# Performance work log

Hardware: AMD Instinct MI355X
Metric: run time of the kernel (lower is better)

## Reference

```python
import jax, jax.numpy as jnp
import numpy as np

E, D, A = 1024, 1024, 512

def setup_inputs() -> dict:
    key = jax.random.key(0)
    ks = jax.random.split(key, 8)
    B, S = 32, 2048
    s_e = 1.0 / np.sqrt(E)
    s_d = 1.0 / np.sqrt(D)
    s_a = 1.0 / np.sqrt(A)
    return {
        "encoder_outputs": jax.random.normal(ks[0], (B, S, E), jnp.float32),
        "decoder_hidden": jax.random.normal(ks[1], (B, D), jnp.float32),
        "We": jax.random.uniform(ks[2], (E, A), jnp.float32, -s_e, s_e),
        "be": jax.random.uniform(ks[3], (A,), jnp.float32, -s_e, s_e),
        "Wd": jax.random.uniform(ks[4], (D, A), jnp.float32, -s_d, s_d),
        "bd": jax.random.uniform(ks[5], (A,), jnp.float32, -s_d, s_d),
        "v_w": jax.random.uniform(ks[6], (A,), jnp.float32, -s_a, s_a),
        "v_b": jax.random.uniform(ks[7], (), jnp.float32, -s_a, s_a),
    }

def reference(encoder_outputs, decoder_hidden, We, be, Wd, bd, v_w, v_b):
    # encoder_energy: [B,S,A]; decoder_energy: [B,1,A]
    enc_e = jnp.einsum('bse,ea->bsa', encoder_outputs, We) + be
    dec_e = (decoder_hidden @ Wd + bd)[:, None, :]
    energy = jnp.tanh(enc_e + dec_e)                     # [B,S,A]
    scores = jnp.einsum('bsa,a->bs', energy, v_w) + v_b  # [B,S]
    attn = jax.nn.softmax(scores, axis=1)                # [B,S]
    context = jnp.einsum('bs,bse->be', attn, encoder_outputs)  # [B,E]
    return context, attn
```

## Files before the change

### kernel.cpp

```cpp
#include <hip/hip_runtime.h>
#include <math.h>

#define E_DIM 1024
#define D_DIM 1024
#define A_DIM 512
#define B_NUM 32
#define S_DIM 2048
#define M_DIM (B_NUM * S_DIM)

typedef unsigned short ushort;
typedef short short8 __attribute__((ext_vector_type(8)));
typedef float f32x4 __attribute__((ext_vector_type(4)));
typedef unsigned short ushort4v __attribute__((ext_vector_type(4)));
typedef unsigned int uint2v __attribute__((ext_vector_type(2)));

typedef const void __attribute__((address_space(1))) cglobal_t;
typedef void __attribute__((address_space(3))) lds_t;

__device__ __forceinline__ void gload_lds16(const void* g, void* l) {
    __builtin_amdgcn_global_load_lds((cglobal_t*)g, (lds_t*)l, 16, 0, 0);
}

__device__ __forceinline__ ushort f2bf(float x) {
    unsigned u = __float_as_uint(x);
    u += 0x7FFF + ((u >> 16) & 1);
    return (ushort)(u >> 16);
}

__device__ __forceinline__ unsigned cvt_pk_bf16(float lo, float hi) {
    unsigned r;
    asm("v_cvt_pk_bf16_f32 %0, %1, %2" : "=v"(r) : "v"(lo), "v"(hi));
    return r;
}

__device__ __forceinline__ float fast_tanh(float x) {
    const float e = __expf(2.0f * x);
    return 1.0f - 2.0f * __builtin_amdgcn_rcpf(e + 1.0f);
}

__global__ __launch_bounds__(256) void k0_dec_energy(
    const float* __restrict__ dh, const float* __restrict__ Wd,
    const float* __restrict__ bd, const float* __restrict__ be,
    float* __restrict__ dec2) {
    __shared__ float sdh[D_DIM];
    const int b = blockIdx.y;
    const int t = threadIdx.x;
    for (int i = t; i < D_DIM; i += 256) sdh[i] = dh[b * D_DIM + i];
    __syncthreads();
    const int a = blockIdx.x * 256 + t;
    float acc = bd[a] + be[a];
#pragma unroll 8
    for (int e = 0; e < D_DIM; ++e) acc += sdh[e] * Wd[(size_t)e * A_DIM + a];
    dec2[b * A_DIM + a] = acc;
}

__global__ __launch_bounds__(256) void k0b_cvt_we(
    const float* __restrict__ We, ushort* __restrict__ Wt) {
    const int n = blockIdx.x;
    const int k0 = threadIdx.x * 4;
    ushort4v v;
#pragma unroll
    for (int j = 0; j < 4; ++j) v[j] = f2bf(We[(size_t)(k0 + j) * A_DIM + n]);
    *reinterpret_cast<ushort4v*>(&Wt[(size_t)n * E_DIM + k0]) = v;
}

#define BM5 128
#define BN5 128
#define NT5 32

__global__ __launch_bounds__(256, 3) void k1_fused(
    const float* __restrict__ enc, const ushort* __restrict__ Wt,
    const float* __restrict__ dec2, const float* __restrict__ v_w,
    float* __restrict__ pscores) {
    __shared__ ushort L[2 * 8192];

    const int t = threadIdx.x;
    const int l = t & 63;
    const int w = t >> 6;
    const int wm = w >> 1, wn = w & 1;
    const int fr = l & 15;
    const int kg = l >> 4;

    const int o = ((blockIdx.x & 7) << 8) | (blockIdx.x >> 3);
    const int x = o >> 2, y = o & 3;
    const int row0 = x * BM5;
    const int n0 = y * BN5;
    const int b = row0 >> 11;

    const int arow = t >> 3;
    const int achk = t & 7;
    const float* AsrcT = enc + (size_t)(row0 + arow) * E_DIM + achk * 4;
    const int aswzc = ((((achk >> 1) ^ ((t >> 4) & 3)) << 4) | ((t & 1) << 3));
    const int awbase = arow * 64 + aswzc;

    const ushort* BsrcQ[2];
#pragma unroll
    for (int q = 0; q < 2; ++q) {
        const int row = q * 64 + w * 16 + (l >> 2);
        const int c = (l & 3) ^ ((row >> 1) & 3);
        BsrcQ[q] = Wt + (size_t)(n0 + row) * E_DIM + c * 8;
    }

    f32x4 acc[4][4];
#pragma unroll
    for (int i = 0; i < 4; ++i)
#pragma unroll
        for (int j = 0; j < 4; ++j) acc[i][j] = (f32x4){0.f, 0.f, 0.f, 0.f};

    float4 pa[4];

#define LOADA5(ktv)                                                            \
    {                                                                          \
        _Pragma("unroll") for (int q = 0; q < 4; ++q)                          \
            pa[q] = *reinterpret_cast<const float4*>(                          \
                AsrcT + (size_t)q * 32 * E_DIM + (ktv) * 32);                  \
    }

#define STAGEB5(cb, ktv)                                                       \
    {                                                                          \
        _Pragma("unroll") for (int q = 0; q < 2; ++q)                          \
            gload_lds16(BsrcQ[q] + (ktv) * 32,                                 \
                        L + (cb) * 8192 + 4096 + (q * 64 + w * 16) * 32);      \
    }

#define WRITEA5(cb)                                                            \
    {                                                                          \
        _Pragma("unroll") for (int q = 0; q < 4; ++q) {                        \
            uint2v v2;                                                         \
            v2[0] = cvt_pk_bf16(pa[q].x, pa[q].y);                             \
            v2[1] = cvt_pk_bf16(pa[q].z, pa[q].w);                             \
            *reinterpret_cast<uint2v*>(                                        \
                (char*)L + (cb) * 16384 + q * 2048 + awbase) = v2;             \
        }                                                                      \
    }

#define WAITV(n) asm volatile("s_waitcnt vmcnt(" #n ")" ::: "memory")

    LOADA5(0);
    STAGEB5(0, 0);
    WAITV(2);
    WRITEA5(0);
    __syncthreads();

    for (int kt = 0; kt < NT5; ++kt) {
        const int cur = kt & 1;

        if (kt < NT5 - 1) {
            LOADA5(kt + 1);
            STAGEB5(cur ^ 1, kt + 1);
        }

        const char* Ab = (const char*)L + cur * 16384;
        const char* Bb = Ab + 8192;
        short8 af[4], bf[4];
#pragma unroll
        for (int i = 0; i < 4; ++i) {
            const int r = wm * 64 + i * 16 + fr;
            af[i] = *reinterpret_cast<const short8*>(
                Ab + r * 64 + ((kg ^ ((r >> 1) & 3)) << 4));
        }
#pragma unroll
        for (int j = 0; j < 4; ++j) {
            const int r = wn * 64 + j * 16 + fr;
            bf[j] = *reinterpret_cast<const short8*>(
                Bb + r * 64 + ((kg ^ ((r >> 1) & 3)) << 4));
        }
        __builtin_amdgcn_s_setprio(1);
#pragma unroll
        for (int i = 0; i < 4; ++i)
#pragma unroll
            for (int j = 0; j < 4; ++j)
                acc[i][j] = __builtin_amdgcn_mfma_f32_16x16x32_bf16(af[i], bf[j], acc[i][j], 0, 0, 0);
        __builtin_amdgcn_s_setprio(0);

        if (kt < NT5 - 1) {
            WAITV(2);
            WRITEA5(cur ^ 1);
        }
        __syncthreads();
    }

    float rowsum[4][4];
#pragma unroll
    for (int i = 0; i < 4; ++i)
#pragma unroll
        for (int r = 0; r < 4; ++r) rowsum[i][r] = 0.0f;

#pragma unroll
    for (int j = 0; j < 4; ++j) {
        const int ag = n0 + wn * 64 + j * 16 + fr;
        const float bias = dec2[b * A_DIM + ag];
        const float vw = v_w[ag];
#pragma unroll
        for (int i = 0; i < 4; ++i)
#pragma unroll
            for (int r = 0; r < 4; ++r)
                rowsum[i][r] += fast_tanh(acc[i][j][r] + bias) * vw;
    }
#pragma unroll
    for (int m = 1; m < 16; m <<= 1)
#pragma unroll
        for (int i = 0; i < 4; ++i)
#pragma unroll
            for (int r = 0; r < 4; ++r)
                rowsum[i][r] += __shfl_xor(rowsum[i][r], m, 64);

    __syncthreads();
    float* red = reinterpret_cast<float*>(L);
    if (fr == 0) {
#pragma unroll
        for (int i = 0; i < 4; ++i)
#pragma unroll
            for (int r = 0; r < 4; ++r)
                red[(wm * 64 + i * 16 + kg * 4 + r) * 2 + wn] = rowsum[i][r];
    }
    __syncthreads();
    if (t < BM5)
        pscores[(size_t)(row0 + t) * 4 + y] = red[t * 2] + red[t * 2 + 1];
}

__global__ __launch_bounds__(256) void k2_softmax(
    const float* __restrict__ pscores, const float* __restrict__ v_b,
    float* __restrict__ attn_out, int W) {
    __shared__ float sc[S_DIM];
    __shared__ float red[8];
    const int b = blockIdx.x;
    const int t = threadIdx.x;
    const int wave = t >> 6, lane = t & 63;
    const float vb = v_b[0];

    float lmax = -1e30f;
    for (int s = t; s < S_DIM; s += 256) {
        float v = vb;
        for (int c = 0; c < W; ++c) v += pscores[(size_t)(b * S_DIM + s) * W + c];
        sc[s] = v;
        lmax = fmaxf(lmax, v);
    }
#pragma unroll
    for (int off = 32; off > 0; off >>= 1) lmax = fmaxf(lmax, __shfl_down(lmax, off, 64));
    if (lane == 0) red[wave] = lmax;
    __syncthreads();
    const float bmax = fmaxf(fmaxf(red[0], red[1]), fmaxf(red[2], red[3]));

    float lsum = 0.0f;
    for (int s = t; s < S_DIM; s += 256) {
        const float e = expf(sc[s] - bmax);
        sc[s] = e;
        lsum += e;
    }
#pragma unroll
    for (int off = 32; off > 0; off >>= 1) lsum += __shfl_down(lsum, off, 64);
    if (lane == 0) red[4 + wave] = lsum;
    __syncthreads();
    const float inv = 1.0f / (red[4] + red[5] + red[6] + red[7]);
    for (int s = t; s < S_DIM; s += 256) attn_out[b * S_DIM + s] = sc[s] * inv;
}

#define SC_CHUNK 128
#define N_SC (S_DIM / SC_CHUNK)
__global__ __launch_bounds__(256) void k3_ctx_partial(
    const float* __restrict__ enc, const float* __restrict__ attn,
    float* __restrict__ pctx) {
    const int b = blockIdx.y;
    const int scb = blockIdx.x;
    const int t = threadIdx.x;
    const int s0 = scb * SC_CHUNK;
    float4 acc = {0.0f, 0.0f, 0.0f, 0.0f};
    const float4* encv =
        reinterpret_cast<const float4*>(enc + (size_t)(b * S_DIM + s0) * E_DIM);
#pragma unroll 4
    for (int s = 0; s < SC_CHUNK; ++s) {
        const float w = attn[b * S_DIM + s0 + s];
        const float4 v = encv[(size_t)s * (E_DIM / 4) + t];
        acc.x += w * v.x;
        acc.y += w * v.y;
        acc.z += w * v.z;
        acc.w += w * v.w;
    }
    *reinterpret_cast<float4*>(&pctx[(size_t)(b * N_SC + scb) * E_DIM + t * 4]) = acc;
}

__global__ __launch_bounds__(256) void k4_ctx_reduce(
    const float* __restrict__ pctx, float* __restrict__ ctx) {
    const int b = blockIdx.x;
    const int t = threadIdx.x;
    float4 acc = {0.0f, 0.0f, 0.0f, 0.0f};
#pragma unroll
    for (int s = 0; s < N_SC; ++s) {
        const float4 v = *reinterpret_cast<const float4*>(
            &pctx[(size_t)(b * N_SC + s) * E_DIM + t * 4]);
        acc.x += v.x;
        acc.y += v.y;
        acc.z += v.z;
        acc.w += v.w;
    }
    *reinterpret_cast<float4*>(&ctx[(size_t)b * E_DIM + t * 4]) = acc;
}

extern "C" void kernel_launch(void* const* d_in, const int* in_sizes, int n_in,
                              void* d_out, int out_size, void* d_ws, size_t ws_size,
                              hipStream_t stream) {
    (void)in_sizes; (void)n_in; (void)out_size; (void)ws_size;
    const float* enc = (const float*)d_in[0];
    const float* dh  = (const float*)d_in[1];
    const float* We  = (const float*)d_in[2];
    const float* be  = (const float*)d_in[3];
    const float* Wd  = (const float*)d_in[4];
    const float* bd  = (const float*)d_in[5];
    const float* vw  = (const float*)d_in[6];
    const float* vb  = (const float*)d_in[7];

    float* out = (float*)d_out;
    float* ctx_out = out;
    float* attn_out = out + B_NUM * E_DIM;

    float* ws = (float*)d_ws;
    float* dec2    = ws;
    float* pscores = ws + 16384;
    float* pctx    = ws + 16384 + 262144;
    ushort* Wt     = (ushort*)(ws + 16384 + 262144 + 524288);

    k0_dec_energy<<<dim3(2, 32), 256, 0, stream>>>(dh, Wd, bd, be, dec2);
    k0b_cvt_we<<<dim3(A_DIM), 256, 0, stream>>>(We, Wt);
    k1_fused<<<dim3((M_DIM / BM5) * (A_DIM / BN5)), 256, 0, stream>>>(
        enc, Wt, dec2, vw, pscores);
    k2_softmax<<<dim3(B_NUM), 256, 0, stream>>>(pscores, vb, attn_out, 4);
    k3_ctx_partial<<<dim3(N_SC, B_NUM), 256, 0, stream>>>(enc, attn_out, pctx);
    k4_ctx_reduce<<<dim3(B_NUM), 256, 0, stream>>>(pctx, ctx_out);
}
```

Baseline: 228.0 us.

## Enlarge fused GEMM tile to 256x256 with triple-buffered phased pipeline

Replaces the 128x128, 256-thread fused energy GEMM with a 256x256 tile run by 512 threads (8 waves). It adds triple-buffered LDS and a two-phase schedule that interleaves global loads, LDS writes and MFMA halves between barriers. The larger tile halves how often the fp32 encoder rows are re-read across N tiles, and the pipeline is meant to hide load latency. In exchange the kernel uses more registers and LDS per block, gets fewer blocks, and relies on hand-placed waitcnt and barriers that could be fragile.

```diff
diff --git a/kernel.cpp b/kernel.cpp
--- a/kernel.cpp
+++ b/kernel.cpp
@@ -64,125 +64,161 @@
     *reinterpret_cast<ushort4v*>(&Wt[(size_t)n * E_DIM + k0]) = v;
 }
 
-#define BM5 128
-#define BN5 128
-#define NT5 32
-
-__global__ __launch_bounds__(256, 3) void k1_fused(
+#define BM6 256
+#define BN6 256
+#define NT6 32
+#define BUFB 32768
+
+__global__ __launch_bounds__(512, 2) void k1_8ph(
     const float* __restrict__ enc, const ushort* __restrict__ Wt,
     const float* __restrict__ dec2, const float* __restrict__ v_w,
     float* __restrict__ pscores) {
-    __shared__ ushort L[2 * 8192];
+    __shared__ ushort L[3 * BUFB / 2];
 
     const int t = threadIdx.x;
     const int l = t & 63;
     const int w = t >> 6;
-    const int wm = w >> 1, wn = w & 1;
+    const int wm = w >> 2, wn = w & 3;
     const int fr = l & 15;
     const int kg = l >> 4;
 
-    const int o = ((blockIdx.x & 7) << 8) | (blockIdx.x >> 3);
-    const int x = o >> 2, y = o & 3;
-    const int row0 = x * BM5;
-    const int n0 = y * BN5;
+    const int o = ((blockIdx.x & 7) << 6) | (blockIdx.x >> 3);
+    const int x = o >> 1, ny = o & 1;
+    const int row0 = x * BM6;
+    const int n0 = ny * BN6;
     const int b = row0 >> 11;
 
-    const int arow = t >> 3;
-    const int achk = t & 7;
-    const float* AsrcT = enc + (size_t)(row0 + arow) * E_DIM + achk * 4;
-    const int aswzc = ((((achk >> 1) ^ ((t >> 4) & 3)) << 4) | ((t & 1) << 3));
-    const int awbase = arow * 64 + aswzc;
+    const float* AsrcT = enc + (size_t)(row0 + (t >> 3)) * E_DIM + (t & 7) * 4;
+    const int aswzc = (((((t & 7) >> 1) ^ ((t >> 4) & 3)) << 4) | ((t & 1) << 3));
+    const int awbase = (t >> 3) * 64 + aswzc;
 
     const ushort* BsrcQ[2];
 #pragma unroll
     for (int q = 0; q < 2; ++q) {
-        const int row = q * 64 + w * 16 + (l >> 2);
+        const int row = q * 128 + w * 16 + (l >> 2);
         const int c = (l & 3) ^ ((row >> 1) & 3);
         BsrcQ[q] = Wt + (size_t)(n0 + row) * E_DIM + c * 8;
     }
 
-    f32x4 acc[4][4];
-#pragma unroll
-    for (int i = 0; i < 4; ++i)
+    f32x4 acc[8][4];
+#pragma unroll
+    for (int i = 0; i < 8; ++i)
 #pragma unroll
         for (int j = 0; j < 4; ++j) acc[i][j] = (f32x4){0.f, 0.f, 0.f, 0.f};
 
-    float4 pa[4];
-
-#define LOADA5(ktv)                                                            \
+    float4 paA[4], paB[4];
+    const int foff = (kg ^ ((fr >> 1) & 3)) << 4;
+
+#define LOADA6(pa, ktv)                                                        \
     {                                                                          \
         _Pragma("unroll") for (int q = 0; q < 4; ++q)                          \
             pa[q] = *reinterpret_cast<const float4*>(                          \
-                AsrcT + (size_t)q * 32 * E_DIM + (ktv) * 32);                  \
-    }
-
-#define STAGEB5(cb, ktv)                                                       \
+                AsrcT + (size_t)q * 64 * E_DIM + (ktv) * 32);                  \
+    }
+
+#define STAGEB6(cb, ktv)                                                       \
     {                                                                          \
         _Pragma("unroll") for (int q = 0; q < 2; ++q)                          \
             gload_lds16(BsrcQ[q] + (ktv) * 32,                                 \
-                        L + (cb) * 8192 + 4096 + (q * 64 + w * 16) * 32);      \
-    }
-
-#define WRITEA5(cb)                                                            \
+                        (char*)L + (cb) + 16384 + q * 8192 + w * 1024);        \
+    }
+
+#define WRITEA6(cb, pa)                                                        \
     {                                                                          \
         _Pragma("unroll") for (int q = 0; q < 4; ++q) {                        \
             uint2v v2;                                                         \
             v2[0] = cvt_pk_bf16(pa[q].x, pa[q].y);                             \
             v2[1] = cvt_pk_bf16(pa[q].z, pa[q].w);                             \
-            *reinterpret_cast<uint2v*>(                                        \
-                (char*)L + (cb) * 16384 + q * 2048 + awbase) = v2;             \
+            *reinterpret_cast<uint2v*>((char*)L + (cb) + q * 4096 + awbase) = v2; \
         }                                                                      \
     }
 
+#define READ_AF03(cb)                                                          \
+    _Pragma("unroll") for (int i = 0; i < 4; ++i)                              \
+        af[i] = *reinterpret_cast<const short8*>(                              \
+            (char*)L + (cb) + (wm * 128 + i * 16 + fr) * 64 + foff);
+#define READ_AF47(cb)                                                          \
+    _Pragma("unroll") for (int i = 0; i < 4; ++i)                              \
+        af[i] = *reinterpret_cast<const short8*>(                              \
+            (char*)L + (cb) + (wm * 128 + (i + 4) * 16 + fr) * 64 + foff);
+#define READ_BF(cb)                                                            \
+    _Pragma("unroll") for (int j = 0; j < 4; ++j)                              \
+        bf[j] = *reinterpret_cast<const short8*>(                              \
+            (char*)L + (cb) + 16384 + (wn * 64 + j * 16 + fr) * 64 + foff);
+#define MFMA16(ibase)                                                          \
+    __builtin_amdgcn_s_setprio(1);                                             \
+    _Pragma("unroll") for (int i = 0; i < 4; ++i)                              \
+        _Pragma("unroll") for (int j = 0; j < 4; ++j)                          \
+            acc[(ibase) + i][j] = __builtin_amdgcn_mfma_f32_16x16x32_bf16(     \
+                af[i], bf[j], acc[(ibase) + i][j], 0, 0, 0);                   \
+    __builtin_amdgcn_s_setprio(0);
+
 #define WAITV(n) asm volatile("s_waitcnt vmcnt(" #n ")" ::: "memory")
-
-    LOADA5(0);
-    STAGEB5(0, 0);
+#define WAITLG() asm volatile("s_waitcnt lgkmcnt(0)" ::: "memory")
+#define BAR() __builtin_amdgcn_s_barrier()
+
+    LOADA6(paA, 0);
+    STAGEB6(0, 0);
     WAITV(2);
-    WRITEA5(0);
-    __syncthreads();
-
-    for (int kt = 0; kt < NT5; ++kt) {
-        const int cur = kt & 1;
-
-        if (kt < NT5 - 1) {
-            LOADA5(kt + 1);
-            STAGEB5(cur ^ 1, kt + 1);
-        }
-
-        const char* Ab = (const char*)L + cur * 16384;
-        const char* Bb = Ab + 8192;
-        short8 af[4], bf[4];
-#pragma unroll
-        for (int i = 0; i < 4; ++i) {
-            const int r = wm * 64 + i * 16 + fr;
-            af[i] = *reinterpret_cast<const short8*>(
-                Ab + r * 64 + ((kg ^ ((r >> 1) & 3)) << 4));
-        }
-#pragma unroll
-        for (int j = 0; j < 4; ++j) {
-            const int r = wn * 64 + j * 16 + fr;
-            bf[j] = *reinterpret_cast<const short8*>(
-                Bb + r * 64 + ((kg ^ ((r >> 1) & 3)) << 4));
-        }
-        __builtin_amdgcn_s_setprio(1);
-#pragma unroll
-        for (int i = 0; i < 4; ++i)
-#pragma unroll
-            for (int j = 0; j < 4; ++j)
-                acc[i][j] = __builtin_amdgcn_mfma_f32_16x16x32_bf16(af[i], bf[j], acc[i][j], 0, 0, 0);
-        __builtin_amdgcn_s_setprio(0);
-
-        if (kt < NT5 - 1) {
-            WAITV(2);
-            WRITEA5(cur ^ 1);
-        }
-        __syncthreads();
-    }
-
-    float rowsum[4][4];
-#pragma unroll
-    for (int i = 0; i < 4; ++i)
+    WRITEA6(0, paA);
+    LOADA6(paB, 1);
+    STAGEB6(BUFB, 1);
+    WAITV(6);
+    WAITLG();
+    BAR();
+
+    int cb0 = 0, cb1 = BUFB, cb2 = 2 * BUFB;
+    short8 af[4], bf[4];
+
+#define TILE(ktv, paCur, paNxt)                                                \
+    {                                                                          \
+                                                                       \
+        READ_AF03(cb0);                                                        \
+        READ_BF(cb0);                                                          \
+        LOADA6(paNxt, (ktv) + 2);                                              \
+        BAR();                                                                 \
+        MFMA16(0);                                                             \
+        BAR();                                                                 \
+                                                                       \
+        READ_AF47(cb0);                                                        \
+        STAGEB6(cb2, (ktv) + 2);                                               \
+        WAITV(8);                                      \
+        WRITEA6(cb1, paCur);                           \
+        WAITLG();                       \
+        BAR();                                                                 \
+        MFMA16(4);                                                             \
+        WAITV(6);                                       \
+        BAR();                                                                 \
+        const int tmp = cb0; cb0 = cb1; cb1 = cb2; cb2 = tmp;                  \
+    }
+
+    for (int tp = 0; tp < 30; tp += 2) {
+        TILE(tp, paB, paA);
+        TILE(tp + 1, paA, paB);
+    }
+    {
+        READ_AF03(cb0); READ_BF(cb0);
+        BAR(); MFMA16(0); BAR();
+        READ_AF47(cb0);
+        WAITV(2);
+        WRITEA6(cb1, paB);
+        WAITLG();
+        BAR(); MFMA16(4);
+        WAITV(0);
+        BAR();
+        const int tmp = cb0; cb0 = cb1; cb1 = cb2; cb2 = tmp;
+    }
+    {
+        READ_AF03(cb0); READ_BF(cb0);
+        BAR(); MFMA16(0); BAR();
+        READ_AF47(cb0);
+        WAITLG();
+        BAR(); MFMA16(4); BAR();
+    }
+
+    float rowsum[8][4];
+#pragma unroll
+    for (int i = 0; i < 8; ++i)
 #pragma unroll
         for (int r = 0; r < 4; ++r) rowsum[i][r] = 0.0f;
 
@@ -192,7 +228,7 @@
         const float bias = dec2[b * A_DIM + ag];
         const float vw = v_w[ag];
 #pragma unroll
-        for (int i = 0; i < 4; ++i)
+        for (int i = 0; i < 8; ++i)
 #pragma unroll
             for (int r = 0; r < 4; ++r)
                 rowsum[i][r] += fast_tanh(acc[i][j][r] + bias) * vw;
@@ -200,7 +236,7 @@
 #pragma unroll
     for (int m = 1; m < 16; m <<= 1)
 #pragma unroll
-        for (int i = 0; i < 4; ++i)
+        for (int i = 0; i < 8; ++i)
 #pragma unroll
             for (int r = 0; r < 4; ++r)
                 rowsum[i][r] += __shfl_xor(rowsum[i][r], m, 64);
@@ -209,14 +245,16 @@
     float* red = reinterpret_cast<float*>(L);
     if (fr == 0) {
 #pragma unroll
-        for (int i = 0; i < 4; ++i)
+        for (int i = 0; i < 8; ++i)
 #pragma unroll
             for (int r = 0; r < 4; ++r)
-                red[(wm * 64 + i * 16 + kg * 4 + r) * 2 + wn] = rowsum[i][r];
-    }
-    __syncthreads();
-    if (t < BM5)
-        pscores[(size_t)(row0 + t) * 4 + y] = red[t * 2] + red[t * 2 + 1];
+                red[(wm * 128 + i * 16 + kg * 4 + r) * 4 + wn] = rowsum[i][r];
+    }
+    __syncthreads();
+    if (t < BM6) {
+        const float s = red[t * 4] + red[t * 4 + 1] + red[t * 4 + 2] + red[t * 4 + 3];
+        pscores[(size_t)(row0 + t) * 2 + ny] = s;
+    }
 }
 
 __global__ __launch_bounds__(256) void k2_softmax(
@@ -317,14 +355,14 @@
     float* ws = (float*)d_ws;
     float* dec2    = ws;
     float* pscores = ws + 16384;
-    float* pctx    = ws + 16384 + 262144;
-    ushort* Wt     = (ushort*)(ws + 16384 + 262144 + 524288);
+    float* pctx    = ws + 16384 + 131072;
+    ushort* Wt     = (ushort*)(ws + 16384 + 131072 + 524288);
 
     k0_dec_energy<<<dim3(2, 32), 256, 0, stream>>>(dh, Wd, bd, be, dec2);
     k0b_cvt_we<<<dim3(A_DIM), 256, 0, stream>>>(We, Wt);
-    k1_fused<<<dim3((M_DIM / BM5) * (A_DIM / BN5)), 256, 0, stream>>>(
+    k1_8ph<<<dim3((M_DIM / BM6) * (A_DIM / BN6)), 512, 0, stream>>>(
         enc, Wt, dec2, vw, pscores);
-    k2_softmax<<<dim3(B_NUM), 256, 0, stream>>>(pscores, vb, attn_out, 4);
+    k2_softmax<<<dim3(B_NUM), 256, 0, stream>>>(pscores, vb, attn_out, 2);
     k3_ctx_partial<<<dim3(N_SC, B_NUM), 256, 0, stream>>>(enc, attn_out, pctx);
     k4_ctx_reduce<<<dim3(B_NUM), 256, 0, stream>>>(pctx, ctx_out);
 }
```

After: 214.9 us. 1.06x faster.
